# Kernel optimization log

Hardware: AMD Instinct MI355X
Metric: run time of the kernel (lower is better)

Reference implementation:

```python
import jax, jax.numpy as jnp
import numpy as np

N = 100000
E = 3200000
IN_DIM, HID_DIM, OUT_DIM = 29, 64, 2


def setup_inputs() -> dict:
    key = jax.random.key(0)
    k1, k2, k3, k4, k5 = jax.random.split(key, 5)
    x = jax.random.normal(k1, (N, IN_DIM), dtype=jnp.float32)
    edge_index = jax.random.randint(k2, (2, E), 0, N, dtype=jnp.int64)
    # GCNConv params: glorot-ish weights, zero bias (bias added after aggregation)
    W1 = jax.random.normal(k3, (IN_DIM, HID_DIM), dtype=jnp.float32) * (1.0 / np.sqrt(IN_DIM))
    b1 = jnp.zeros((HID_DIM,), dtype=jnp.float32)
    W2 = jax.random.normal(k4, (HID_DIM, OUT_DIM), dtype=jnp.float32) * (1.0 / np.sqrt(HID_DIM))
    b2 = jnp.zeros((OUT_DIM,), dtype=jnp.float32)
    return {"x": x, "edge_index": edge_index, "W1": W1, "b1": b1, "W2": W2, "b2": b2}


def _gcn_norm(edge_index, n_nodes):
    # PyG gcn_norm with add_self_loops=True, symmetric D^-1/2 A D^-1/2
    loop = jnp.arange(n_nodes, dtype=edge_index.dtype)
    src = jnp.concatenate([edge_index[0], loop])
    dst = jnp.concatenate([edge_index[1], loop])
    deg = jax.ops.segment_sum(jnp.ones_like(dst, dtype=jnp.float32), dst, num_segments=n_nodes)
    dinv = jnp.where(deg > 0, jax.lax.rsqrt(deg), 0.0)
    norm = dinv[src] * dinv[dst]  # [E + N]
    return src, dst, norm


def _gcn_conv(x, src, dst, norm, W, b):
    h = x @ W                      # [N, d_out] -- transform first (smaller msgs)
    msg = h[src] * norm[:, None]   # [E+N, d_out] gather + scale
    out = jax.ops.segment_sum(msg, dst, num_segments=x.shape[0])  # scatter-add
    return out + b


def reference(x, edge_index, W1, b1, W2, b2):
    src, dst, norm = _gcn_norm(edge_index, x.shape[0])
    h = _gcn_conv(x, src, dst, norm, W1, b1)
    h = jax.nn.relu(h)
    out = _gcn_conv(h, src, dst, norm, W2, b2)
    return out
```

## Files before the change

### kernel.cpp

```cpp
#include <hip/hip_runtime.h>

#define N_NODES 100000
#define N_EDGES 3200000
#define IN_DIM  29
#define HID_DIM 64
#define NBUCK   391
#define BNODES  256
#define CAP     10240
#define EPT     8
#define EPB     4096

#define OFF_CUR   0
#define OFF_ROWS  512
#define OFF_ROWE  100512
#define OFF_DINV  200512
#define OFF_ZS    300512
#define OFF_EBUF  500544
#define OFF_XS    4504384

static __device__ __forceinline__ unsigned short f2bf(float f) {
    unsigned u = __float_as_uint(f);
    u += 0x7fffu + ((u >> 16) & 1u);
    return (unsigned short)(u >> 16);
}

static __device__ __forceinline__ void unpack_add(float4& acc, uint2 a) {
    acc.x += __uint_as_float(a.x << 16);
    acc.y += __uint_as_float(a.x & 0xFFFF0000u);
    acc.z += __uint_as_float(a.y << 16);
    acc.w += __uint_as_float(a.y & 0xFFFF0000u);
}

__global__ __launch_bounds__(512) void partition_kernel(const int* __restrict__ ei,
        int* __restrict__ gcursor, int* __restrict__ ebuf) {
    __shared__ int lhist[NBUCK];
    __shared__ int lcur[NBUCK];
    int tid = threadIdx.x;
    for (int i = tid; i < NBUCK; i += 512) lhist[i] = 0;
    __syncthreads();

    int base = blockIdx.x * EPB + tid * EPT;
    int dv[EPT], sv[EPT];
    bool valid = (base < N_EDGES);
    if (valid) {
        const int4* dp = (const int4*)(ei + N_EDGES + base);
        const int4* sp = (const int4*)(ei + base);
        #pragma unroll
        for (int q = 0; q < 2; ++q) {
            int4 t = dp[q];
            dv[4*q+0] = t.x; dv[4*q+1] = t.y; dv[4*q+2] = t.z; dv[4*q+3] = t.w;
            int4 u = sp[q];
            sv[4*q+0] = u.x; sv[4*q+1] = u.y; sv[4*q+2] = u.z; sv[4*q+3] = u.w;
        }
        #pragma unroll
        for (int j = 0; j < EPT; ++j) atomicAdd(&lhist[dv[j] >> 8], 1);
    }
    __syncthreads();
    for (int i = tid; i < NBUCK; i += 512) {
        int c = lhist[i];
        lcur[i] = c ? (atomicAdd(&gcursor[i], c) + i * CAP) : 0;
    }
    __syncthreads();
    if (valid) {
        #pragma unroll
        for (int j = 0; j < EPT; ++j) {
            int d = dv[j];
            int pos = atomicAdd(&lcur[d >> 8], 1);
            ebuf[pos] = sv[j] | ((d & 255) << 17);
        }
    }
}

__global__ __launch_bounds__(1024) void bucketsort_kernel(const int* __restrict__ gcursor,
        int* __restrict__ ebuf, int* __restrict__ rowStart, int* __restrict__ rowEnd,
        float* __restrict__ dinv, const float* __restrict__ x,
        unsigned int* __restrict__ xsb, float* __restrict__ zs) {
    __shared__ int   cnt[BNODES];
    __shared__ int   cur[BNODES];
    __shared__ float dls[BNODES];
    __shared__ int   stage[CAP];
    __shared__ int   szp_sh;
    int b = blockIdx.x, tid = threadIdx.x;
    if (tid < BNODES) cnt[tid] = 0;
    __syncthreads();
    int base = b * CAP;
    int size = gcursor[b];

    for (int j = tid; j < size; j += 1024)
        atomicAdd(&cnt[((unsigned)ebuf[base + j]) >> 17], 1);
    __syncthreads();

    int v = 0, vp = 0;
    if (tid < BNODES) { v = cnt[tid]; vp = (v + 7) & ~7; cur[tid] = vp; }
    __syncthreads();
    for (int off = 1; off < BNODES; off <<= 1) {
        int t = 0;
        if (tid < BNODES && tid >= off) t = cur[tid - off];
        __syncthreads();
        if (tid < BNODES) cur[tid] += t;
        __syncthreads();
    }
    if (tid < BNODES) {
        int excl = cur[tid] - vp;
        int node = b * BNODES + tid;
        if (node < N_NODES) {
            rowStart[node] = base + excl;
            rowEnd[node]   = base + excl + vp;
            float dn = rsqrtf((float)v + 1.0f);
            dinv[node] = dn;
            dls[tid] = dn;
        }
        if (tid == BNODES - 1) szp_sh = cur[tid];
        cur[tid] = excl;
        for (int p2 = excl + v; p2 < excl + vp; ++p2)
            stage[p2] = N_NODES;
    }
    __syncthreads();

    for (int j = tid; j < size; j += 1024) {
        unsigned p = (unsigned)ebuf[base + j];
        int pos = atomicAdd(&cur[p >> 17], 1);
        stage[pos] = p & 0x1FFFF;
    }
    __syncthreads();
    int szp = szp_sh;
    for (int j = tid; j < szp; j += 1024)
        ebuf[base + j] = stage[j];

    for (int i = tid; i < BNODES * 16; i += 1024) {
        int dl = i >> 4, kp = i & 15;
        int nd = b * BNODES + dl;
        if (nd < N_NODES) {
            float dn = dls[dl];
            int k0 = kp * 2, k1 = k0 + 1;
            float f0 = (k0 < IN_DIM) ? x[nd * IN_DIM + k0] * dn : 0.0f;
            float f1 = (k1 < IN_DIM) ? x[nd * IN_DIM + k1] * dn : 0.0f;
            unsigned u = (unsigned)f2bf(f0) | ((unsigned)f2bf(f1) << 16);
            xsb[(size_t)nd * 16 + kp] = u;
        } else if (nd == N_NODES) {
            xsb[(size_t)nd * 16 + kp] = 0u;
        }
    }
    if (b == 0 && tid == 0) {
        zs[2 * N_NODES]     = 0.0f;
        zs[2 * N_NODES + 1] = 0.0f;
    }
}

#define XROW(i) (((unsigned)(i) << 6) | moff)

#define PREP(P, rs, re, node)                                            \
    int P##i0, P##i1, P##i2, P##i3, P##i4, P##i5;                        \
    {                                                                    \
        int relim = max((re) - 1, (rs));                                 \
        int j0 = (rs) + q;                                               \
        int t0 = ebuf[min(j0,      relim)];                              \
        int t1 = ebuf[min(j0 + 8,  relim)];                              \
        int t2 = ebuf[min(j0 + 16, relim)];                              \
        int t3 = ebuf[min(j0 + 24, relim)];                              \
        int t4 = ebuf[min(j0 + 32, relim)];                              \
        P##i0 = (j0      < (re)) ? t0 : N_NODES;                         \
        P##i1 = (j0 + 8  < (re)) ? t1 : N_NODES;                         \
        P##i2 = (j0 + 16 < (re)) ? t2 : N_NODES;                         \
        P##i3 = (j0 + 24 < (re)) ? t3 : N_NODES;                         \
        P##i4 = (j0 + 32 < (re)) ? t4 : N_NODES;                         \
        P##i5 = (q == 0) ? (node) : N_NODES;    \
    }

#define GATH(G, P)                                                       \
    uint2 G##0 = *(const uint2*)(xb + XROW(P##i0));                      \
    uint2 G##1 = *(const uint2*)(xb + XROW(P##i1));                      \
    uint2 G##2 = *(const uint2*)(xb + XROW(P##i2));                      \
    uint2 G##3 = *(const uint2*)(xb + XROW(P##i3));                      \
    uint2 G##4 = *(const uint2*)(xb + XROW(P##i4));                      \
    uint2 G##5 = *(const uint2*)(xb + XROW(P##i5));

#define UNP(acc, G)                                                      \
    unpack_add(acc, G##0); unpack_add(acc, G##1); unpack_add(acc, G##2); \
    unpack_add(acc, G##3); unpack_add(acc, G##4); unpack_add(acc, G##5);

#define TAIL(acc, rs, re)                                                \
    {                                                                    \
        int j = (rs) + q + 40;                                           \
        while (j < (re)) {                  \
            int s = ebuf[j];                                             \
            uint2 a = *(const uint2*)(xb + XROW(s));                     \
            unpack_add(acc, a);                                          \
            j += 8;                                                      \
        }                                                                \
    }

static __device__ __forceinline__ void mlp_store(float4 acc, int node, int lane,
        const float* w1s, const float* b1s, const float* w2s,
        const float* __restrict__ dinv, float* __restrict__ zs) {
    #pragma unroll
    for (int msk = 8; msk <= 32; msk <<= 1) {
        acc.x += __shfl_xor(acc.x, msk);
        acc.y += __shfl_xor(acc.y, msk);
        acc.z += __shfl_xor(acc.z, msk);
        acc.w += __shfl_xor(acc.w, msk);
    }
    float dn = dinv[node];
    acc.x *= dn; acc.y *= dn; acc.z *= dn; acc.w *= dn;

    float h = b1s[lane];
    #pragma unroll
    for (int kk = 0; kk < IN_DIM; ++kk) {
        float comp = ((kk & 3) == 0) ? acc.x : ((kk & 3) == 1) ? acc.y
                   : ((kk & 3) == 2) ? acc.z : acc.w;
        h = fmaf(__shfl(comp, kk >> 2), w1s[kk * HID_DIM + lane], h);
    }
    h = fmaxf(h, 0.0f);

    float z0 = h * w2s[lane * 2 + 0];
    float z1 = h * w2s[lane * 2 + 1];
    #pragma unroll
    for (int off = 32; off > 0; off >>= 1) {
        z0 += __shfl_down(z0, off);
        z1 += __shfl_down(z1, off);
    }
    if (lane == 0) {
        float2 o; o.x = z0 * dn; o.y = z1 * dn;
        *(float2*)(zs + node * 2) = o;
    }
}

__global__ __launch_bounds__(256) void fused_kernel(const unsigned int* __restrict__ xs_,
        const int* __restrict__ rowStart, const int* __restrict__ rowEnd,
        const int* __restrict__ ebuf, const float* __restrict__ dinv,
        const float* __restrict__ W1, const float* __restrict__ b1,
        const float* __restrict__ W2, float* __restrict__ zs) {
    __shared__ float w1s[IN_DIM * HID_DIM];
    __shared__ float b1s[HID_DIM];
    __shared__ float w2s[HID_DIM * 2];
    const int tid = threadIdx.x;
    for (int i = tid; i < IN_DIM * HID_DIM; i += 256) w1s[i] = W1[i];
    if (tid < HID_DIM) {
        b1s[tid] = b1[tid];
        w2s[tid * 2 + 0] = W2[tid * 2 + 0];
        w2s[tid * 2 + 1] = W2[tid * 2 + 1];
    }
    __syncthreads();

    const int lane = tid & 63;
    const int q = lane >> 3, m = lane & 7;
    const unsigned moff = (unsigned)(m << 3);
    const char* xb = (const char*)xs_;
    const int n0 = blockIdx.x * 16 + (tid >> 6) * 4;

    const int rs0 = rowStart[n0+0], re0 = rowEnd[n0+0];
    const int rs1 = rowStart[n0+1], re1 = rowEnd[n0+1];
    const int rs2 = rowStart[n0+2], re2 = rowEnd[n0+2];
    const int rs3 = rowStart[n0+3], re3 = rowEnd[n0+3];

    PREP(pa, rs0, re0, n0+0)
    GATH(ga, pa)
    PREP(pb, rs1, re1, n0+1)
    float4 acc0 = make_float4(0.f, 0.f, 0.f, 0.f);
    UNP(acc0, ga)
    TAIL(acc0, rs0, re0)
    GATH(gb, pb)
    PREP(pc, rs2, re2, n0+2)
    mlp_store(acc0, n0+0, lane, w1s, b1s, w2s, dinv, zs);

    float4 acc1 = make_float4(0.f, 0.f, 0.f, 0.f);
    UNP(acc1, gb)
    TAIL(acc1, rs1, re1)
    GATH(gc, pc)
    PREP(pd, rs3, re3, n0+3)
    mlp_store(acc1, n0+1, lane, w1s, b1s, w2s, dinv, zs);

    float4 acc2 = make_float4(0.f, 0.f, 0.f, 0.f);
    UNP(acc2, gc)
    TAIL(acc2, rs2, re2)
    GATH(gd, pd)
    mlp_store(acc2, n0+2, lane, w1s, b1s, w2s, dinv, zs);

    float4 acc3 = make_float4(0.f, 0.f, 0.f, 0.f);
    UNP(acc3, gd)
    TAIL(acc3, rs3, re3)
    mlp_store(acc3, n0+3, lane, w1s, b1s, w2s, dinv, zs);
}

__global__ __launch_bounds__(256) void agg2_kernel(const float* __restrict__ zs,
        const int* __restrict__ rowStart, const int* __restrict__ rowEnd,
        const int* __restrict__ ebuf, const float* __restrict__ dinv,
        const float* __restrict__ b2, float* __restrict__ out) {
    int tid = threadIdx.x;
    int node = blockIdx.x * 16 + (tid >> 4);
    if (node >= N_NODES) return;
    int gl = tid & 15;
    const float2* zs2 = (const float2*)zs;
    float a0 = 0.0f, a1 = 0.0f, c0 = 0.0f, c1 = 0.0f;
    int rs = rowStart[node], re = rowEnd[node];
    int j = rs + gl;
    for (; j + 16 < re; j += 32) {
        float2 za = zs2[ebuf[j]];
        float2 zb = zs2[ebuf[j + 16]];
        a0 += za.x; a1 += za.y;
        c0 += zb.x; c1 += zb.y;
    }
    if (j < re) {
        float2 za = zs2[ebuf[j]];
        a0 += za.x; a1 += za.y;
    }
    a0 += c0; a1 += c1;
    a0 += __shfl_xor(a0, 8); a1 += __shfl_xor(a1, 8);
    a0 += __shfl_xor(a0, 4); a1 += __shfl_xor(a1, 4);
    a0 += __shfl_xor(a0, 2); a1 += __shfl_xor(a1, 2);
    a0 += __shfl_xor(a0, 1); a1 += __shfl_xor(a1, 1);
    if (gl == 0) {
        float dn = dinv[node];
        float2 zself = zs2[node];
        float2 o;
        o.x = dn * (a0 + zself.x) + b2[0];
        o.y = dn * (a1 + zself.y) + b2[1];
        ((float2*)out)[node] = o;
    }
}

extern "C" void kernel_launch(void* const* d_in, const int* in_sizes, int n_in,
                              void* d_out, int out_size, void* d_ws, size_t ws_size,
                              hipStream_t stream) {
    const float* x  = (const float*)d_in[0];
    const int*   ei = (const int*)d_in[1];
    const float* W1 = (const float*)d_in[2];
    const float* b1 = (const float*)d_in[3];
    const float* W2 = (const float*)d_in[4];
    const float* b2 = (const float*)d_in[5];
    float* out = (float*)d_out;

    int*   wsi      = (int*)d_ws;
    float* wsf      = (float*)d_ws;
    int*   gcursor  = wsi + OFF_CUR;
    int*   rowStart = wsi + OFF_ROWS;
    int*   rowEnd   = wsi + OFF_ROWE;
    float* dinv     = wsf + OFF_DINV;
    float* zs       = wsf + OFF_ZS;
    int*   ebuf     = wsi + OFF_EBUF;
    unsigned int* xsb = (unsigned int*)(wsi + OFF_XS);

    hipMemsetAsync(gcursor, 0, NBUCK * sizeof(int), stream);
    partition_kernel<<<(N_EDGES + EPB - 1) / EPB, 512, 0, stream>>>(ei, gcursor, ebuf);
    bucketsort_kernel<<<NBUCK, 1024, 0, stream>>>(gcursor, ebuf, rowStart, rowEnd, dinv, x, xsb, zs);
    fused_kernel<<<N_NODES / 16, 256, 0, stream>>>(xsb, rowStart, rowEnd, ebuf, dinv, W1, b1, W2, zs);
    agg2_kernel<<<N_NODES / 16, 256, 0, stream>>>(zs, rowStart, rowEnd, ebuf, dinv, b2, out);
}
```

Baseline: 216.4 us.

## Replace two-pass bucket partition with degree-count CSR build via global atomics

Replaces the partition and shared-memory bucket sort with three kernels. One counts in-degrees with global atomics, one scans each 256-node bucket to set row offsets, dinv and the bf16 features, and one places source indices into the padded CSR with per-node atomic cursors. This drops the staged intermediate pass over the edge buffer and the large LDS bucket sort. In exchange it performs 6.4M scattered global atomics, reads edge_index twice, and leaves the order of edges within each row nondeterministic. The degree array shares storage with zs, which is only written later.

```diff
diff --git a/kernel.cpp b/kernel.cpp
--- a/kernel.cpp
+++ b/kernel.cpp
@@ -10,13 +10,14 @@
 #define EPT     8
 #define EPB     4096
 
-#define OFF_CUR   0
-#define OFF_ROWS  512
-#define OFF_ROWE  100512
-#define OFF_DINV  200512
-#define OFF_ZS    300512
-#define OFF_EBUF  500544
-#define OFF_XS    4504384
+#define OFF_ZS    0
+#define OFF_DEG   0
+#define OFF_CURG  100000
+#define OFF_ROWS  200064
+#define OFF_ROWE  300064
+#define OFF_DINV  400064
+#define OFF_EBUF  500096
+#define OFF_XS    4503936
 
 static __device__ __forceinline__ unsigned short f2bf(float f) {
     unsigned u = __float_as_uint(f);
@@ -31,112 +32,61 @@
     acc.w += __uint_as_float(a.y & 0xFFFF0000u);
 }
 
-__global__ __launch_bounds__(512) void partition_kernel(const int* __restrict__ ei,
-        int* __restrict__ gcursor, int* __restrict__ ebuf) {
-    __shared__ int lhist[NBUCK];
-    __shared__ int lcur[NBUCK];
-    int tid = threadIdx.x;
-    for (int i = tid; i < NBUCK; i += 512) lhist[i] = 0;
-    __syncthreads();
-
-    int base = blockIdx.x * EPB + tid * EPT;
-    int dv[EPT], sv[EPT];
-    bool valid = (base < N_EDGES);
-    if (valid) {
-        const int4* dp = (const int4*)(ei + N_EDGES + base);
-        const int4* sp = (const int4*)(ei + base);
-        #pragma unroll
-        for (int q = 0; q < 2; ++q) {
-            int4 t = dp[q];
-            dv[4*q+0] = t.x; dv[4*q+1] = t.y; dv[4*q+2] = t.z; dv[4*q+3] = t.w;
-            int4 u = sp[q];
-            sv[4*q+0] = u.x; sv[4*q+1] = u.y; sv[4*q+2] = u.z; sv[4*q+3] = u.w;
-        }
-        #pragma unroll
-        for (int j = 0; j < EPT; ++j) atomicAdd(&lhist[dv[j] >> 8], 1);
-    }
-    __syncthreads();
-    for (int i = tid; i < NBUCK; i += 512) {
-        int c = lhist[i];
-        lcur[i] = c ? (atomicAdd(&gcursor[i], c) + i * CAP) : 0;
-    }
-    __syncthreads();
-    if (valid) {
-        #pragma unroll
-        for (int j = 0; j < EPT; ++j) {
-            int d = dv[j];
-            int pos = atomicAdd(&lcur[d >> 8], 1);
-            ebuf[pos] = sv[j] | ((d & 255) << 17);
-        }
-    }
-}
-
-__global__ __launch_bounds__(1024) void bucketsort_kernel(const int* __restrict__ gcursor,
-        int* __restrict__ ebuf, int* __restrict__ rowStart, int* __restrict__ rowEnd,
+__global__ __launch_bounds__(512) void count_kernel(const int* __restrict__ ei,
+        int* __restrict__ deg) {
+    int base = blockIdx.x * EPB + threadIdx.x * EPT;
+    if (base >= N_EDGES) return;
+    const int4* dp = (const int4*)(ei + N_EDGES + base);
+    #pragma unroll
+    for (int q2 = 0; q2 < 2; ++q2) {
+        int4 t = dp[q2];
+        atomicAdd(&deg[t.x], 1); atomicAdd(&deg[t.y], 1);
+        atomicAdd(&deg[t.z], 1); atomicAdd(&deg[t.w], 1);
+    }
+}
+
+__global__ __launch_bounds__(256) void setup_kernel(const int* __restrict__ deg,
+        int* __restrict__ curg, int* __restrict__ rowStart, int* __restrict__ rowEnd,
         float* __restrict__ dinv, const float* __restrict__ x,
-        unsigned int* __restrict__ xsb, float* __restrict__ zs) {
-    __shared__ int   cnt[BNODES];
-    __shared__ int   cur[BNODES];
+        unsigned int* __restrict__ xsb, int* __restrict__ ebuf,
+        float* __restrict__ zs) {
+    __shared__ int   sc[BNODES];
     __shared__ float dls[BNODES];
-    __shared__ int   stage[CAP];
-    __shared__ int   szp_sh;
     int b = blockIdx.x, tid = threadIdx.x;
-    if (tid < BNODES) cnt[tid] = 0;
-    __syncthreads();
-    int base = b * CAP;
-    int size = gcursor[b];
-
-    for (int j = tid; j < size; j += 1024)
-        atomicAdd(&cnt[((unsigned)ebuf[base + j]) >> 17], 1);
-    __syncthreads();
-
-    int v = 0, vp = 0;
-    if (tid < BNODES) { v = cnt[tid]; vp = (v + 7) & ~7; cur[tid] = vp; }
+    int node = b * BNODES + tid;
+    int v  = (node < N_NODES) ? deg[node] : 0;
+    int vp = (v + 7) & ~7;
+    sc[tid] = vp;
     __syncthreads();
     for (int off = 1; off < BNODES; off <<= 1) {
-        int t = 0;
-        if (tid < BNODES && tid >= off) t = cur[tid - off];
+        int t = (tid >= off) ? sc[tid - off] : 0;
         __syncthreads();
-        if (tid < BNODES) cur[tid] += t;
+        sc[tid] += t;
         __syncthreads();
     }
-    if (tid < BNODES) {
-        int excl = cur[tid] - vp;
-        int node = b * BNODES + tid;
-        if (node < N_NODES) {
-            rowStart[node] = base + excl;
-            rowEnd[node]   = base + excl + vp;
-            float dn = rsqrtf((float)v + 1.0f);
-            dinv[node] = dn;
-            dls[tid] = dn;
-        }
-        if (tid == BNODES - 1) szp_sh = cur[tid];
-        cur[tid] = excl;
-        for (int p2 = excl + v; p2 < excl + vp; ++p2)
-            stage[p2] = N_NODES;
-    }
+    int excl = sc[tid] - vp;
+    int base = b * CAP;
+    float dn = rsqrtf((float)v + 1.0f);
+    if (node < N_NODES) {
+        rowStart[node] = base + excl;
+        rowEnd[node]   = base + excl + vp;
+        dinv[node]     = dn;
+        curg[node]     = base + excl;
+        for (int p = v; p < vp; ++p)
+            ebuf[base + excl + p] = N_NODES;
+    }
+    dls[tid] = dn;
     __syncthreads();
 
-    for (int j = tid; j < size; j += 1024) {
-        unsigned p = (unsigned)ebuf[base + j];
-        int pos = atomicAdd(&cur[p >> 17], 1);
-        stage[pos] = p & 0x1FFFF;
-    }
-    __syncthreads();
-    int szp = szp_sh;
-    for (int j = tid; j < szp; j += 1024)
-        ebuf[base + j] = stage[j];
-
-    for (int i = tid; i < BNODES * 16; i += 1024) {
+    for (int i = tid; i < BNODES * 16; i += 256) {
         int dl = i >> 4, kp = i & 15;
         int nd = b * BNODES + dl;
         if (nd < N_NODES) {
-            float dn = dls[dl];
+            float d2 = dls[dl];
             int k0 = kp * 2, k1 = k0 + 1;
-            float f0 = (k0 < IN_DIM) ? x[nd * IN_DIM + k0] * dn : 0.0f;
-            float f1 = (k1 < IN_DIM) ? x[nd * IN_DIM + k1] * dn : 0.0f;
-            unsigned u = (unsigned)f2bf(f0) | ((unsigned)f2bf(f1) << 16);
-            xsb[(size_t)nd * 16 + kp] = u;
+            float f0 = (k0 < IN_DIM) ? x[nd * IN_DIM + k0] * d2 : 0.0f;
+            float f1 = (k1 < IN_DIM) ? x[nd * IN_DIM + k1] * d2 : 0.0f;
+            xsb[(size_t)nd * 16 + kp] = (unsigned)f2bf(f0) | ((unsigned)f2bf(f1) << 16);
         } else if (nd == N_NODES) {
             xsb[(size_t)nd * 16 + kp] = 0u;
         }
@@ -144,6 +94,24 @@
     if (b == 0 && tid == 0) {
         zs[2 * N_NODES]     = 0.0f;
         zs[2 * N_NODES + 1] = 0.0f;
+    }
+}
+
+__global__ __launch_bounds__(512) void place_kernel(const int* __restrict__ ei,
+        int* __restrict__ curg, int* __restrict__ ebuf) {
+    int base = blockIdx.x * EPB + threadIdx.x * EPT;
+    if (base >= N_EDGES) return;
+    const int4* sp = (const int4*)(ei + base);
+    const int4* dp = (const int4*)(ei + N_EDGES + base);
+    #pragma unroll
+    for (int q2 = 0; q2 < 2; ++q2) {
+        int4 s = sp[q2];
+        int4 d = dp[q2];
+        int p0 = atomicAdd(&curg[d.x], 1);
+        int p1 = atomicAdd(&curg[d.y], 1);
+        int p2 = atomicAdd(&curg[d.z], 1);
+        int p3 = atomicAdd(&curg[d.w], 1);
+        ebuf[p0] = s.x; ebuf[p1] = s.y; ebuf[p2] = s.z; ebuf[p3] = s.w;
     }
 }
 
@@ -332,17 +300,20 @@
 
     int*   wsi      = (int*)d_ws;
     float* wsf      = (float*)d_ws;
-    int*   gcursor  = wsi + OFF_CUR;
+    float* zs       = wsf + OFF_ZS;
+    int*   deg      = wsi + OFF_DEG;
+    int*   curg     = wsi + OFF_CURG;
     int*   rowStart = wsi + OFF_ROWS;
     int*   rowEnd   = wsi + OFF_ROWE;
     float* dinv     = wsf + OFF_DINV;
-    float* zs       = wsf + OFF_ZS;
     int*   ebuf     = wsi + OFF_EBUF;
     unsigned int* xsb = (unsigned int*)(wsi + OFF_XS);
 
-    hipMemsetAsync(gcursor, 0, NBUCK * sizeof(int), stream);
-    partition_kernel<<<(N_EDGES + EPB - 1) / EPB, 512, 0, stream>>>(ei, gcursor, ebuf);
-    bucketsort_kernel<<<NBUCK, 1024, 0, stream>>>(gcursor, ebuf, rowStart, rowEnd, dinv, x, xsb, zs);
+    int egrid = (N_EDGES + EPB - 1) / EPB;
+    hipMemsetAsync(deg, 0, N_NODES * sizeof(int), stream);
+    count_kernel<<<egrid, 512, 0, stream>>>(ei, deg);
+    setup_kernel<<<NBUCK, 256, 0, stream>>>(deg, curg, rowStart, rowEnd, dinv, x, xsb, ebuf, zs);
+    place_kernel<<<egrid, 512, 0, stream>>>(ei, curg, ebuf);
     fused_kernel<<<N_NODES / 16, 256, 0, stream>>>(xsb, rowStart, rowEnd, ebuf, dinv, W1, b1, W2, zs);
-    agg2_kernel<<<N_NODES / 16, 256, 0, stream>>>(zs, rowStart, rowEnd, ebuf, dinv, b2, out);
-}
+    agg2_kernel<<<(N_NODES + 15) / 16, 256, 0, stream>>>(zs, rowStart, rowEnd, ebuf, dinv, b2, out);
+}
```

New measurement: 600.6 us. 178% more time.

## Compute degrees with global atomics and split bucket sort into setup and placement kernels

Applied to the files above, without the earlier changes.

Per-node in-degree is now counted in the partition kernel with global atomics, so the bucket sort no longer needs its own histogram pass. The old bucketsort kernel is split in two. A 256-thread setup kernel does the prefix scan, writes row ranges and dinv, and builds the bf16 scaled features. A placement kernel then scatters edges into their slots in shared memory. The aim is to take the feature conversion and counting off the 1024-thread, shared-memory-heavy blocks. In exchange it adds 3.2M global atomics, an extra memset and an extra kernel launch. The deg array reuses the zs offset, which is safe only because zs is written later.

```diff
diff --git a/kernel.cpp b/kernel.cpp
--- a/kernel.cpp
+++ b/kernel.cpp
@@ -15,6 +15,7 @@
 #define OFF_ROWE  100512
 #define OFF_DINV  200512
 #define OFF_ZS    300512
+#define OFF_DEG   300512
 #define OFF_EBUF  500544
 #define OFF_XS    4504384
 
@@ -32,7 +33,7 @@
 }
 
 __global__ __launch_bounds__(512) void partition_kernel(const int* __restrict__ ei,
-        int* __restrict__ gcursor, int* __restrict__ ebuf) {
+        int* __restrict__ gcursor, int* __restrict__ ebuf, int* __restrict__ deg) {
     __shared__ int lhist[NBUCK];
     __shared__ int lcur[NBUCK];
     int tid = threadIdx.x;
@@ -53,7 +54,10 @@
             sv[4*q+0] = u.x; sv[4*q+1] = u.y; sv[4*q+2] = u.z; sv[4*q+3] = u.w;
         }
         #pragma unroll
-        for (int j = 0; j < EPT; ++j) atomicAdd(&lhist[dv[j] >> 8], 1);
+        for (int j = 0; j < EPT; ++j) {
+            atomicAdd(&lhist[dv[j] >> 8], 1);
+            atomicAdd(&deg[dv[j]], 1);
+        }
     }
     __syncthreads();
     for (int i = tid; i < NBUCK; i += 512) {
@@ -71,80 +75,78 @@
     }
 }
 
-__global__ __launch_bounds__(1024) void bucketsort_kernel(const int* __restrict__ gcursor,
-        int* __restrict__ ebuf, int* __restrict__ rowStart, int* __restrict__ rowEnd,
+__global__ __launch_bounds__(256) void setup_kernel(const int* __restrict__ deg,
+        int* __restrict__ rowStart, int* __restrict__ rowEnd,
         float* __restrict__ dinv, const float* __restrict__ x,
         unsigned int* __restrict__ xsb, float* __restrict__ zs) {
-    __shared__ int   cnt[BNODES];
-    __shared__ int   cur[BNODES];
+    __shared__ int   sc[BNODES];
     __shared__ float dls[BNODES];
-    __shared__ int   stage[CAP];
-    __shared__ int   szp_sh;
     int b = blockIdx.x, tid = threadIdx.x;
-    if (tid < BNODES) cnt[tid] = 0;
-    __syncthreads();
+    int node = b * BNODES + tid;
+    int v  = (node < N_NODES) ? deg[node] : 0;
+    int vp = (v + 7) & ~7;
+    sc[tid] = vp;
+    __syncthreads();
+    for (int off = 1; off < BNODES; off <<= 1) {
+        int t = (tid >= off) ? sc[tid - off] : 0;
+        __syncthreads();
+        sc[tid] += t;
+        __syncthreads();
+    }
+    int excl = sc[tid] - vp;
+    int base = b * CAP;
+    float dn = rsqrtf((float)v + 1.0f);
+    if (node < N_NODES) {
+        rowStart[node] = base + excl;
+        rowEnd[node]   = base + excl + vp;
+        dinv[node]     = dn;
+    }
+    dls[tid] = dn;
+    __syncthreads();
+
+    for (int i = tid; i < BNODES * 16; i += 256) {
+        int dl = i >> 4, kp = i & 15;
+        int nd = b * BNODES + dl;
+        if (nd < N_NODES) {
+            float d2 = dls[dl];
+            int k0 = kp * 2, k1 = k0 + 1;
+            float f0 = (k0 < IN_DIM) ? x[nd * IN_DIM + k0] * d2 : 0.0f;
+            float f1 = (k1 < IN_DIM) ? x[nd * IN_DIM + k1] * d2 : 0.0f;
+            xsb[(size_t)nd * 16 + kp] = (unsigned)f2bf(f0) | ((unsigned)f2bf(f1) << 16);
+        } else if (nd == N_NODES) {
+            xsb[(size_t)nd * 16 + kp] = 0u;
+        }
+    }
+    if (b == 0 && tid == 0) {
+        zs[2 * N_NODES]     = 0.0f;
+        zs[2 * N_NODES + 1] = 0.0f;
+    }
+}
+
+__global__ __launch_bounds__(1024) void placeb_kernel(const int* __restrict__ gcursor,
+        const int* __restrict__ rowStart, const int* __restrict__ rowEnd,
+        int* __restrict__ ebuf) {
+    __shared__ int cur[BNODES];
+    __shared__ int stage[CAP];
+    int b = blockIdx.x, tid = threadIdx.x;
     int base = b * CAP;
     int size = gcursor[b];
-
-    for (int j = tid; j < size; j += 1024)
-        atomicAdd(&cnt[((unsigned)ebuf[base + j]) >> 17], 1);
-    __syncthreads();
-
-    int v = 0, vp = 0;
-    if (tid < BNODES) { v = cnt[tid]; vp = (v + 7) & ~7; cur[tid] = vp; }
-    __syncthreads();
-    for (int off = 1; off < BNODES; off <<= 1) {
-        int t = 0;
-        if (tid < BNODES && tid >= off) t = cur[tid - off];
-        __syncthreads();
-        if (tid < BNODES) cur[tid] += t;
-        __syncthreads();
-    }
+    int lastnode = min(b * BNODES + BNODES - 1, N_NODES - 1);
+    int szp = rowEnd[lastnode] - base;
     if (tid < BNODES) {
-        int excl = cur[tid] - vp;
         int node = b * BNODES + tid;
-        if (node < N_NODES) {
-            rowStart[node] = base + excl;
-            rowEnd[node]   = base + excl + vp;
-            float dn = rsqrtf((float)v + 1.0f);
-            dinv[node] = dn;
-            dls[tid] = dn;
-        }
-        if (tid == BNODES - 1) szp_sh = cur[tid];
-        cur[tid] = excl;
-        for (int p2 = excl + v; p2 < excl + vp; ++p2)
-            stage[p2] = N_NODES;
-    }
-    __syncthreads();
-
+        cur[tid] = (node < N_NODES) ? rowStart[node] - base : 0;
+    }
+    for (int j = tid; j < szp; j += 1024) stage[j] = N_NODES;
+    __syncthreads();
     for (int j = tid; j < size; j += 1024) {
         unsigned p = (unsigned)ebuf[base + j];
         int pos = atomicAdd(&cur[p >> 17], 1);
         stage[pos] = p & 0x1FFFF;
     }
     __syncthreads();
-    int szp = szp_sh;
     for (int j = tid; j < szp; j += 1024)
         ebuf[base + j] = stage[j];
-
-    for (int i = tid; i < BNODES * 16; i += 1024) {
-        int dl = i >> 4, kp = i & 15;
-        int nd = b * BNODES + dl;
-        if (nd < N_NODES) {
-            float dn = dls[dl];
-            int k0 = kp * 2, k1 = k0 + 1;
-            float f0 = (k0 < IN_DIM) ? x[nd * IN_DIM + k0] * dn : 0.0f;
-            float f1 = (k1 < IN_DIM) ? x[nd * IN_DIM + k1] * dn : 0.0f;
-            unsigned u = (unsigned)f2bf(f0) | ((unsigned)f2bf(f1) << 16);
-            xsb[(size_t)nd * 16 + kp] = u;
-        } else if (nd == N_NODES) {
-            xsb[(size_t)nd * 16 + kp] = 0u;
-        }
-    }
-    if (b == 0 && tid == 0) {
-        zs[2 * N_NODES]     = 0.0f;
-        zs[2 * N_NODES + 1] = 0.0f;
-    }
 }
 
 #define XROW(i) (((unsigned)(i) << 6) | moff)
@@ -337,12 +339,15 @@
     int*   rowEnd   = wsi + OFF_ROWE;
     float* dinv     = wsf + OFF_DINV;
     float* zs       = wsf + OFF_ZS;
+    int*   deg      = wsi + OFF_DEG;
     int*   ebuf     = wsi + OFF_EBUF;
     unsigned int* xsb = (unsigned int*)(wsi + OFF_XS);
 
     hipMemsetAsync(gcursor, 0, NBUCK * sizeof(int), stream);
-    partition_kernel<<<(N_EDGES + EPB - 1) / EPB, 512, 0, stream>>>(ei, gcursor, ebuf);
-    bucketsort_kernel<<<NBUCK, 1024, 0, stream>>>(gcursor, ebuf, rowStart, rowEnd, dinv, x, xsb, zs);
+    hipMemsetAsync(deg, 0, N_NODES * sizeof(int), stream);
+    partition_kernel<<<(N_EDGES + EPB - 1) / EPB, 512, 0, stream>>>(ei, gcursor, ebuf, deg);
+    setup_kernel<<<NBUCK, 256, 0, stream>>>(deg, rowStart, rowEnd, dinv, x, xsb, zs);
+    placeb_kernel<<<NBUCK, 1024, 0, stream>>>(gcursor, rowStart, rowEnd, ebuf);
     fused_kernel<<<N_NODES / 16, 256, 0, stream>>>(xsb, rowStart, rowEnd, ebuf, dinv, W1, b1, W2, zs);
-    agg2_kernel<<<N_NODES / 16, 256, 0, stream>>>(zs, rowStart, rowEnd, ebuf, dinv, b2, out);
-}
+    agg2_kernel<<<(N_NODES + 15) / 16, 256, 0, stream>>>(zs, rowStart, rowEnd, ebuf, dinv, b2, out);
+}
```

After: 339.5 us. 1.57x slower.

## Stage partitioned edges in LDS and write padded buckets with coalesced stores

Applied to the files above, without the earlier changes.

The partition kernel now processes 16K edges per 1024-thread block. It computes a local prefix sum over buckets, scatters the packed edges into shared memory, and then copies each bucket to global memory as a contiguous run padded to 16 entries with -1 sentinels. This replaces scattered per-edge global writes with coalesced bucket writes and reduces global atomics per block. The bucket sort kernel now skips the sentinels. The cost is a much larger LDS footprint (about 89KB), which lowers occupancy, and a larger per-bucket capacity to absorb the padding.

```diff
diff --git a/kernel.cpp b/kernel.cpp
--- a/kernel.cpp
+++ b/kernel.cpp
@@ -6,9 +6,10 @@
 #define HID_DIM 64
 #define NBUCK   391
 #define BNODES  256
-#define CAP     10240
-#define EPT     8
-#define EPB     4096
+#define CAP     10496
+#define PEPT    16
+#define PEPB    16384
+#define PSTAGE  22272
 
 #define OFF_CUR   0
 #define OFF_ROWS  512
@@ -16,7 +17,7 @@
 #define OFF_DINV  200512
 #define OFF_ZS    300512
 #define OFF_EBUF  500544
-#define OFF_XS    4504384
+#define OFF_XS    4604480
 
 static __device__ __forceinline__ unsigned short f2bf(float f) {
     unsigned u = __float_as_uint(f);
@@ -31,43 +32,74 @@
     acc.w += __uint_as_float(a.y & 0xFFFF0000u);
 }
 
-__global__ __launch_bounds__(512) void partition_kernel(const int* __restrict__ ei,
+__global__ __launch_bounds__(1024) void partition_kernel(const int* __restrict__ ei,
         int* __restrict__ gcursor, int* __restrict__ ebuf) {
     __shared__ int lhist[NBUCK];
     __shared__ int lcur[NBUCK];
+    __shared__ int gbase[NBUCK];
+    __shared__ int soff[NBUCK];
+    __shared__ int sc[NBUCK];
+    __shared__ int stage[PSTAGE];
     int tid = threadIdx.x;
-    for (int i = tid; i < NBUCK; i += 512) lhist[i] = 0;
-    __syncthreads();
-
-    int base = blockIdx.x * EPB + tid * EPT;
-    int dv[EPT], sv[EPT];
+    for (int i = tid; i < NBUCK; i += 1024) lhist[i] = 0;
+    __syncthreads();
+
+    int base = blockIdx.x * PEPB + tid * PEPT;
     bool valid = (base < N_EDGES);
+    if (valid) {
+        const int4* dp = (const int4*)(ei + N_EDGES + base);
+        #pragma unroll
+        for (int q = 0; q < 4; ++q) {
+            int4 t = dp[q];
+            atomicAdd(&lhist[t.x >> 8], 1); atomicAdd(&lhist[t.y >> 8], 1);
+            atomicAdd(&lhist[t.z >> 8], 1); atomicAdd(&lhist[t.w >> 8], 1);
+        }
+    }
+    __syncthreads();
+    int c = 0, p = 0;
+    if (tid < NBUCK) { c = lhist[tid]; p = (c + 15) & ~15; sc[tid] = p; }
+    __syncthreads();
+    for (int off = 1; off < NBUCK; off <<= 1) {
+        int t = 0;
+        if (tid < NBUCK && tid >= off) t = sc[tid - off];
+        __syncthreads();
+        if (tid < NBUCK) sc[tid] += t;
+        __syncthreads();
+    }
+    if (tid < NBUCK) {
+        int so = sc[tid] - p;
+        soff[tid] = so;
+        lcur[tid] = so;
+        gbase[tid] = p ? (tid * CAP + atomicAdd(&gcursor[tid], p)) : 0;
+    }
+    __syncthreads();
     if (valid) {
         const int4* dp = (const int4*)(ei + N_EDGES + base);
         const int4* sp = (const int4*)(ei + base);
         #pragma unroll
-        for (int q = 0; q < 2; ++q) {
-            int4 t = dp[q];
-            dv[4*q+0] = t.x; dv[4*q+1] = t.y; dv[4*q+2] = t.z; dv[4*q+3] = t.w;
-            int4 u = sp[q];
-            sv[4*q+0] = u.x; sv[4*q+1] = u.y; sv[4*q+2] = u.z; sv[4*q+3] = u.w;
-        }
-        #pragma unroll
-        for (int j = 0; j < EPT; ++j) atomicAdd(&lhist[dv[j] >> 8], 1);
-    }
-    __syncthreads();
-    for (int i = tid; i < NBUCK; i += 512) {
-        int c = lhist[i];
-        lcur[i] = c ? (atomicAdd(&gcursor[i], c) + i * CAP) : 0;
-    }
-    __syncthreads();
-    if (valid) {
-        #pragma unroll
-        for (int j = 0; j < EPT; ++j) {
-            int d = dv[j];
-            int pos = atomicAdd(&lcur[d >> 8], 1);
-            ebuf[pos] = sv[j] | ((d & 255) << 17);
-        }
+        for (int q = 0; q < 4; ++q) {
+            int4 d = dp[q];
+            int4 s = sp[q];
+            int pos;
+            pos = atomicAdd(&lcur[d.x >> 8], 1); stage[pos] = s.x | ((d.x & 255) << 17);
+            pos = atomicAdd(&lcur[d.y >> 8], 1); stage[pos] = s.y | ((d.y & 255) << 17);
+            pos = atomicAdd(&lcur[d.z >> 8], 1); stage[pos] = s.z | ((d.z & 255) << 17);
+            pos = atomicAdd(&lcur[d.w >> 8], 1); stage[pos] = s.w | ((d.w & 255) << 17);
+        }
+    }
+    __syncthreads();
+    if (tid < NBUCK) {
+        int endReal = lcur[tid];
+        int endPad  = soff[tid] + (((lhist[tid]) + 15) & ~15);
+        for (int k = endReal; k < endPad; ++k) stage[k] = -1;
+    }
+    __syncthreads();
+    int wv = tid >> 6, ln = tid & 63;
+    for (int b = wv; b < NBUCK; b += 16) {
+        int np = (lhist[b] + 15) & ~15;
+        int so = soff[b], gb = gbase[b];
+        for (int k = ln; k < np; k += 64)
+            ebuf[gb + k] = stage[so + k];
     }
 }
 
@@ -86,8 +118,10 @@
     int base = b * CAP;
     int size = gcursor[b];
 
-    for (int j = tid; j < size; j += 1024)
-        atomicAdd(&cnt[((unsigned)ebuf[base + j]) >> 17], 1);
+    for (int j = tid; j < size; j += 1024) {
+        unsigned p = (unsigned)ebuf[base + j];
+        if (p != 0xFFFFFFFFu) atomicAdd(&cnt[p >> 17], 1);
+    }
     __syncthreads();
 
     int v = 0, vp = 0;
@@ -119,8 +153,10 @@
 
     for (int j = tid; j < size; j += 1024) {
         unsigned p = (unsigned)ebuf[base + j];
-        int pos = atomicAdd(&cur[p >> 17], 1);
-        stage[pos] = p & 0x1FFFF;
+        if (p != 0xFFFFFFFFu) {
+            int pos = atomicAdd(&cur[p >> 17], 1);
+            stage[pos] = p & 0x1FFFF;
+        }
     }
     __syncthreads();
     int szp = szp_sh;
@@ -135,8 +171,7 @@
             int k0 = kp * 2, k1 = k0 + 1;
             float f0 = (k0 < IN_DIM) ? x[nd * IN_DIM + k0] * dn : 0.0f;
             float f1 = (k1 < IN_DIM) ? x[nd * IN_DIM + k1] * dn : 0.0f;
-            unsigned u = (unsigned)f2bf(f0) | ((unsigned)f2bf(f1) << 16);
-            xsb[(size_t)nd * 16 + kp] = u;
+            xsb[(size_t)nd * 16 + kp] = (unsigned)f2bf(f0) | ((unsigned)f2bf(f1) << 16);
         } else if (nd == N_NODES) {
             xsb[(size_t)nd * 16 + kp] = 0u;
         }
@@ -341,8 +376,8 @@
     unsigned int* xsb = (unsigned int*)(wsi + OFF_XS);
 
     hipMemsetAsync(gcursor, 0, NBUCK * sizeof(int), stream);
-    partition_kernel<<<(N_EDGES + EPB - 1) / EPB, 512, 0, stream>>>(ei, gcursor, ebuf);
+    partition_kernel<<<(N_EDGES + PEPB - 1) / PEPB, 1024, 0, stream>>>(ei, gcursor, ebuf);
     bucketsort_kernel<<<NBUCK, 1024, 0, stream>>>(gcursor, ebuf, rowStart, rowEnd, dinv, x, xsb, zs);
     fused_kernel<<<N_NODES / 16, 256, 0, stream>>>(xsb, rowStart, rowEnd, ebuf, dinv, W1, b1, W2, zs);
-    agg2_kernel<<<N_NODES / 16, 256, 0, stream>>>(zs, rowStart, rowEnd, ebuf, dinv, b2, out);
-}
+    agg2_kernel<<<(N_NODES + 15) / 16, 256, 0, stream>>>(zs, rowStart, rowEnd, ebuf, dinv, b2, out);
+}
```

Result: faster. 203.0 us (-6.2%).
